# Kernel optimization log

Hardware: AMD Instinct MI355X
Metric: run time of the kernel (lower is better)

## Reference

```python
import jax, jax.numpy as jnp
import numpy as np

DIM = 1024
NUM_HEADS = 16


def setup_inputs() -> dict:
    key = jax.random.key(0)
    ks = jax.random.split(key, 5)
    B, Nx, Ny = 8, 1024, 1024
    w_std = DIM ** -0.5  # keep logits in a sane range
    x = jax.random.normal(ks[0], (B, Nx, DIM), dtype=jnp.float32)
    y = jax.random.normal(ks[1], (B, Ny, DIM), dtype=jnp.float32)
    Wq = jax.random.normal(ks[2], (DIM, DIM), dtype=jnp.float32) * w_std
    Wk = jax.random.normal(ks[3], (DIM, DIM), dtype=jnp.float32) * w_std
    Wv = jax.random.normal(ks[4], (DIM, DIM), dtype=jnp.float32) * w_std
    return {"x": x, "y": y, "Wq": Wq, "Wk": Wk, "Wv": Wv}


def reference(x, y, Wq, Wk, Wv):
    B, Nx, dim = x.shape
    Ny = y.shape[1]
    H = NUM_HEADS
    hd = dim // H
    scale = jnp.asarray(hd ** 0.5, dtype=x.dtype)

    # torch nn.Linear: out = inp @ W.T
    Q = (x @ Wq.T) / scale                 # [B, Nx, dim]
    K = y @ Wk.T                           # [B, Ny, dim]
    V = y @ Wv.T                           # [B, Ny, dim]

    # split(last, hd) + cat(dim=0) == reshape heads to leading axis
    Qh = Q.reshape(B, Nx, H, hd)
    Kh = K.reshape(B, Ny, H, hd)
    Vh = V.reshape(B, Ny, H, hd)

    logits = jnp.einsum("bqhd,bkhd->bhqk", Qh, Kh)   # [B, H, Nx, Ny]
    A = jax.nn.softmax(logits, axis=-1)
    y_ = jnp.einsum("bhqk,bkhd->bqhd", A, Vh).reshape(B, Nx, dim)

    # second stage: x @ y_^T, scaled, softmax over queries (dim=-2)
    s = jnp.einsum("bqd,bkd->bqk", x, y_) / scale    # [B, Nx, Nx]
    return jax.nn.softmax(s, axis=-2)
```

## Files before the change

### kernel.cpp

```cpp
#include <hip/hip_runtime.h>

typedef unsigned short ushort_t;
typedef __attribute__((ext_vector_type(8))) short short8;
typedef __attribute__((ext_vector_type(4))) float f32x4;
typedef __attribute__((ext_vector_type(2))) unsigned uint2v;
typedef __attribute__((ext_vector_type(4))) unsigned uint4v;

#define DIM 1024
#define BATCH 8
#define NSEQ 1024
#define HEADS 16
#define HD 64

__device__ __forceinline__ ushort_t f2b(float f) {
    union { float f; unsigned u; } v; v.f = f;
    unsigned r = v.u + 0x7FFF + ((v.u >> 16) & 1);
    return (ushort_t)(r >> 16);
}

__device__ __forceinline__ unsigned cvtpk_bf16(float a, float b) {
    unsigned r;
    asm("v_cvt_pk_bf16_f32 %0, %1, %2" : "=v"(r) : "v"(a), "v"(b));
    return r;
}

__device__ __forceinline__ void g2l16(const void* g, void* l) {
    __builtin_amdgcn_global_load_lds(
        (const __attribute__((address_space(1))) void*)g,
        (__attribute__((address_space(3))) void*)l, 16, 0, 0);
}

__global__ __launch_bounds__(256) void conv_all(const float4* __restrict__ x,
                                                const float4* __restrict__ y,
                                                const float4* __restrict__ wq,
                                                const float4* __restrict__ wk,
                                                const float4* __restrict__ wv,
                                                short8* __restrict__ xb,
                                                short8* __restrict__ yb,
                                                short8* __restrict__ wqb,
                                                short8* __restrict__ wkb,
                                                short8* __restrict__ wvb) {
    int j = blockIdx.x;
    const float4* src; short8* dst; int base;
    if (j < 4096)      { src = x;  dst = xb;  base = j; }
    else if (j < 8192) { src = y;  dst = yb;  base = j - 4096; }
    else if (j < 8704) { src = wq; dst = wqb; base = j - 8192; }
    else if (j < 9216) { src = wk; dst = wkb; base = j - 8704; }
    else               { src = wv; dst = wvb; base = j - 9216; }
    int i = base * 256 + threadIdx.x;
    float4 a = src[i * 2], b = src[i * 2 + 1];
    short8 o;
    o[0] = (short)f2b(a.x); o[1] = (short)f2b(a.y);
    o[2] = (short)f2b(a.z); o[3] = (short)f2b(a.w);
    o[4] = (short)f2b(b.x); o[5] = (short)f2b(b.y);
    o[6] = (short)f2b(b.z); o[7] = (short)f2b(b.w);
    dst[i] = o;
}

template <typename OutT, int MODE, bool EXPOUT>
__global__ __launch_bounds__(256) void gemm_nt(const ushort_t* __restrict__ A,
                                               const ushort_t* __restrict__ B,
                                               OutT* __restrict__ C,
                                               long sA, long sB, long sC,
                                               float scale,
                                               float* __restrict__ partial) {
    __shared__ __align__(16) ushort_t As[128 * 64];
    __shared__ __align__(16) ushort_t Bs[128 * 64];
    const int tid = threadIdx.x;
    const int w = tid >> 6, l = tid & 63;
    const int wm = w >> 1, wn = w & 1;
    const int lo = l & 15, hi = l >> 4;

    int bx, by, bz;
    const int j = blockIdx.x;
    if constexpr (MODE == 1) { by = j & 63; bx = j >> 6; bz = 0; }
    else if constexpr (MODE == 2) { bx = j & 7; by = (j >> 3) & 7; bz = j >> 6; }
    else { bz = j & 7; bx = (j >> 3) & 7; by = j >> 6; }

    const long abase = (long)by * 128 * 1024 + (long)bz * sA;
    const long bbase = (long)bx * 128 * 1024 + (long)bz * sB;
    const char* Abytes = (const char*)A;
    const char* Bbytes = (const char*)B;

    f32x4 acc[4][4];
#pragma unroll
    for (int m = 0; m < 4; m++)
#pragma unroll
        for (int n = 0; n < 4; n++) acc[m][n] = (f32x4)0.f;

    for (int kt = 0; kt < 1024; kt += 64) {
#pragma unroll
        for (int i = 0; i < 4; i++) {
            int o16 = tid + i * 256;
            int row = o16 >> 3;
            int cb = (o16 & 7) * 16;
            int scb = cb ^ ((row & 7) << 4);
            g2l16(Abytes + (abase + (long)row * 1024 + kt) * 2 + scb,
                  (char*)As + o16 * 16);
            g2l16(Bbytes + (bbase + (long)row * 1024 + kt) * 2 + scb,
                  (char*)Bs + o16 * 16);
        }
        __syncthreads();
#pragma unroll
        for (int kc = 0; kc < 2; kc++) {
            short8 af[4], bfr[4];
#pragma unroll
            for (int m = 0; m < 4; m++) {
                int row = wm * 64 + m * 16 + lo;
                int cb = (kc * 64 + hi * 16) ^ ((row & 7) << 4);
                af[m] = *(const short8*)((const char*)As + row * 128 + cb);
            }
#pragma unroll
            for (int n = 0; n < 4; n++) {
                int row = wn * 64 + n * 16 + lo;
                int cb = (kc * 64 + hi * 16) ^ ((row & 7) << 4);
                bfr[n] = *(const short8*)((const char*)Bs + row * 128 + cb);
            }
            __builtin_amdgcn_s_setprio(1);
#pragma unroll
            for (int m = 0; m < 4; m++)
#pragma unroll
                for (int n = 0; n < 4; n++)
                    acc[m][n] = __builtin_amdgcn_mfma_f32_16x16x32_bf16(
                        af[m], bfr[n], acc[m][n], 0, 0, 0);
            __builtin_amdgcn_s_setprio(0);
        }
        __syncthreads();
    }

    const long cb0 = (long)bz * sC;
    if constexpr (EXPOUT) {
#pragma unroll
        for (int n = 0; n < 4; n++) {
            float csum = 0.f;
#pragma unroll
            for (int m = 0; m < 4; m++)
#pragma unroll
                for (int r = 0; r < 4; r++) {
                    long row = (long)by * 128 + wm * 64 + m * 16 + hi * 4 + r;
                    long col = (long)bx * 128 + wn * 64 + n * 16 + lo;
                    float e = exp2f(acc[m][n][r] * scale);
                    C[cb0 + row * 1024 + col] = (OutT)e;
                    csum += e;
                }
            csum += __shfl_xor(csum, 16);
            csum += __shfl_xor(csum, 32);
            if (hi == 0)
                partial[((long)bz << 14) + (by * 2 + wm) * 1024 +
                        bx * 128 + wn * 64 + n * 16 + lo] = csum;
        }
    } else {
#pragma unroll
        for (int m = 0; m < 4; m++)
#pragma unroll
            for (int n = 0; n < 4; n++)
#pragma unroll
                for (int r = 0; r < 4; r++) {
                    long row = (long)by * 128 + wm * 64 + m * 16 + hi * 4 + r;
                    long col = (long)bx * 128 + wn * 64 + n * 16 + lo;
                    float v = acc[m][n][r] * scale;
                    if constexpr (sizeof(OutT) == 2)
                        C[cb0 + row * 1024 + col] = (OutT)f2b(v);
                    else
                        C[cb0 + row * 1024 + col] = v;
                }
    }
}

__global__ __launch_bounds__(256, 4) void flash_attn(const ushort_t* __restrict__ Q,
                                                     const ushort_t* __restrict__ Kb,
                                                     const ushort_t* __restrict__ Vt,
                                                     ushort_t* __restrict__ Yo) {
    __shared__ __align__(16) ushort_t Ks[2][64 * 64];
    __shared__ __align__(16) ushort_t Vs[2][64 * 64];
    const int j = blockIdx.x;
    const int g = j & 127, qt = j >> 7;
    const int h = g & 15, b = g >> 4;
    const int tid = threadIdx.x, w = tid >> 6, l = tid & 63;
    const int lo = l & 15, hi = l >> 4;
    const int sw = (lo & 7) << 4;

    const char* Khb = (const char*)(Kb + (long)b * 1024 * 1024 + h * 64);
    const char* Vhb = (const char*)(Vt + (long)b * 1024 * 1024 + (long)h * 64 * 1024);

    const long qrow0 = (long)b * 1024 + qt * 128 + w * 32;
    short8 qf[2][2];
#pragma unroll
    for (int qg = 0; qg < 2; qg++)
#pragma unroll
        for (int dk = 0; dk < 2; dk++)
            qf[qg][dk] = *(const short8*)(Q + (qrow0 + qg * 16 + lo) * 1024 +
                                          h * 64 + dk * 32 + hi * 8);

    float l_sum[2] = {0.f, 0.f};
    f32x4 o_acc[4][2];
#pragma unroll
    for (int ch = 0; ch < 4; ch++)
#pragma unroll
        for (int qg = 0; qg < 2; qg++) o_acc[ch][qg] = (f32x4)0.f;

    {
#pragma unroll
        for (int i = 0; i < 2; i++) {
            int o16 = tid + i * 256;
            int row = o16 >> 3, cb = (o16 & 7) * 16;
            int scb = cb ^ ((row & 7) << 4);
            g2l16(Khb + (long)row * 2048 + scb, (char*)Ks[0] + o16 * 16);
            g2l16(Vhb + (long)row * 2048 + scb, (char*)Vs[0] + o16 * 16);
        }
    }

    for (int t = 0; t < 16; t++) {
        __syncthreads();
        if (t < 15) {
            int kt = (t + 1) * 64;
            int bufn = (t + 1) & 1;
#pragma unroll
            for (int i = 0; i < 2; i++) {
                int o16 = tid + i * 256;
                int row = o16 >> 3, cb = (o16 & 7) * 16;
                int scb = cb ^ ((row & 7) << 4);
                g2l16(Khb + ((long)(kt + row) * 1024) * 2 + scb,
                      (char*)Ks[bufn] + o16 * 16);
                g2l16(Vhb + ((long)row * 1024 + kt) * 2 + scb,
                      (char*)Vs[bufn] + o16 * 16);
            }
        }
        const char* Kc = (const char*)Ks[t & 1];
        const char* Vc = (const char*)Vs[t & 1];

        f32x4 s_acc[4][2];
        __builtin_amdgcn_s_setprio(1);
#pragma unroll
        for (int ks = 0; ks < 4; ks++) {
            const char* kr = Kc + (ks * 16 + lo) * 128;
            short8 kf0 = *(const short8*)(kr + ((hi * 16) ^ sw));
            short8 kf1 = *(const short8*)(kr + ((64 + hi * 16) ^ sw));
#pragma unroll
            for (int qg = 0; qg < 2; qg++) {
                s_acc[ks][qg] = __builtin_amdgcn_mfma_f32_16x16x32_bf16(
                    kf0, qf[qg][0], (f32x4)0.f, 0, 0, 0);
                s_acc[ks][qg] = __builtin_amdgcn_mfma_f32_16x16x32_bf16(
                    kf1, qf[qg][1], s_acc[ks][qg], 0, 0, 0);
            }
        }
        __builtin_amdgcn_s_setprio(0);

        unsigned pk[2][4][2];
#pragma unroll
        for (int qg = 0; qg < 2; qg++) {
            float psk[4];
#pragma unroll
            for (int ks = 0; ks < 4; ks++) {
#pragma unroll
                for (int r = 0; r < 4; r++)
                    s_acc[ks][qg][r] = exp2f(s_acc[ks][qg][r]);
                psk[ks] = (s_acc[ks][qg][0] + s_acc[ks][qg][1]) +
                          (s_acc[ks][qg][2] + s_acc[ks][qg][3]);
                pk[qg][ks][0] = cvtpk_bf16(s_acc[ks][qg][0], s_acc[ks][qg][1]);
                pk[qg][ks][1] = cvtpk_bf16(s_acc[ks][qg][2], s_acc[ks][qg][3]);
            }
            float ps = (psk[0] + psk[1]) + (psk[2] + psk[3]);
            ps += __shfl_xor(ps, 16);
            ps += __shfl_xor(ps, 32);
            l_sum[qg] += ps;
        }

#pragma unroll
        for (int kk = 0; kk < 2; kk++) {
            short8 pa[2];
#pragma unroll
            for (int qg = 0; qg < 2; qg++) {
                unsigned a0 = pk[qg][2 * kk][0], b0 = pk[qg][2 * kk + 1][0];
                uint2v t0 = __builtin_amdgcn_permlane32_swap(a0, b0, false, false);
                t0 = __builtin_amdgcn_permlane16_swap(t0[0], t0[1], false, false);
                unsigned a1 = pk[qg][2 * kk][1], b1 = pk[qg][2 * kk + 1][1];
                uint2v t1 = __builtin_amdgcn_permlane32_swap(a1, b1, false, false);
                t1 = __builtin_amdgcn_permlane16_swap(t1[0], t1[1], false, false);
                union { uint4v u; short8 s; } cv;
                cv.u = (uint4v){t0[0], t1[0], t0[1], t1[1]};
                pa[qg] = cv.s;
            }
            __builtin_amdgcn_s_setprio(1);
#pragma unroll
            for (int ch = 0; ch < 4; ch++) {
                short8 vf = *(const short8*)(Vc + (ch * 16 + lo) * 128 +
                                             ((kk * 64 + hi * 16) ^ sw));
#pragma unroll
                for (int qg = 0; qg < 2; qg++)
                    o_acc[ch][qg] = __builtin_amdgcn_mfma_f32_16x16x32_bf16(
                        pa[qg], vf, o_acc[ch][qg], 0, 0, 0);
            }
            __builtin_amdgcn_s_setprio(0);
        }
    }

    float inv[2][4];
#pragma unroll
    for (int qg = 0; qg < 2; qg++)
#pragma unroll
        for (int r = 0; r < 4; r++)
            inv[qg][r] = 1.f / __shfl(l_sum[qg], hi * 4 + r);
#pragma unroll
    for (int ch = 0; ch < 4; ch++)
#pragma unroll
        for (int qg = 0; qg < 2; qg++)
#pragma unroll
            for (int r = 0; r < 4; r++) {
                long row = qrow0 + qg * 16 + hi * 4 + r;
                Yo[row * 1024 + h * 64 + ch * 16 + lo] =
                    f2b(o_acc[ch][qg][r] * inv[qg][r]);
            }
}

__global__ __launch_bounds__(256) void colsum_inv(const float* __restrict__ partial,
                                                  float* __restrict__ inv) {
    int i = blockIdx.x * 256 + threadIdx.x;
    int b = i >> 10, c = i & 1023;
    const float* p = partial + ((long)b << 14) + c;
    float s = 0.f;
#pragma unroll
    for (int k = 0; k < 16; k++) s += p[k * 1024];
    inv[i] = 1.f / s;
}

__global__ __launch_bounds__(256) void scale_rows(float4* __restrict__ S,
                                                  const float4* __restrict__ inv) {
    long i = (long)blockIdx.x * 256 + threadIdx.x;
    int c4 = (int)(i & 255);
    int b = (int)(i >> 18);
    float4 v = S[i];
    float4 iv = inv[b * 256 + c4];
    v.x *= iv.x; v.y *= iv.y; v.z *= iv.z; v.w *= iv.w;
    S[i] = v;
}

extern "C" void kernel_launch(void* const* d_in, const int* in_sizes, int n_in,
                              void* d_out, int out_size, void* d_ws, size_t ws_size,
                              hipStream_t stream) {
    const float* x = (const float*)d_in[0];
    const float* y = (const float*)d_in[1];
    const float* Wq = (const float*)d_in[2];
    const float* Wk = (const float*)d_in[3];
    const float* Wv = (const float*)d_in[4];
    float* out = (float*)d_out;

    const long NXD = (long)BATCH * NSEQ * DIM;
    const long WSZ = (long)DIM * DIM;
    ushort_t* xb = (ushort_t*)d_ws;
    ushort_t* yb = xb + NXD;
    ushort_t* wqb = yb + NXD;
    ushort_t* wkb = wqb + WSZ;
    ushort_t* wvb = wkb + WSZ;
    ushort_t* Qb = wvb + WSZ;
    ushort_t* Kbb = Qb + NXD;
    ushort_t* Vtb = Kbb + NXD;
    ushort_t* Yob = Vtb + NXD;
    float* partial = (float*)(Yob + NXD);
    float* invcol = partial + 8 * 16 * 1024;

    conv_all<<<9728, 256, 0, stream>>>((const float4*)x, (const float4*)y,
                                       (const float4*)Wq, (const float4*)Wk,
                                       (const float4*)Wv, (short8*)xb, (short8*)yb,
                                       (short8*)wqb, (short8*)wkb, (short8*)wvb);

    gemm_nt<ushort_t, 1, false><<<512, 256, 0, stream>>>(
        xb, wqb, Qb, 0, 0, 0, 0.125f * 1.44269504f, nullptr);
    gemm_nt<ushort_t, 1, false><<<512, 256, 0, stream>>>(
        yb, wkb, Kbb, 0, 0, 0, 1.0f, nullptr);
    gemm_nt<ushort_t, 2, false><<<512, 256, 0, stream>>>(
        wvb, yb, Vtb, 0, WSZ, WSZ, 1.0f, nullptr);
    flash_attn<<<1024, 256, 0, stream>>>(Qb, Kbb, Vtb, Yob);
    gemm_nt<float, 3, true><<<512, 256, 0, stream>>>(
        xb, Yob, out, WSZ, WSZ, WSZ, 0.125f * 1.44269504f, partial);
    colsum_inv<<<32, 256, 0, stream>>>(partial, invcol);
    scale_rows<<<8192, 256, 0, stream>>>((float4*)out, (const float4*)invcol);
}
```

Baseline: 281.5 us.

## Fuse column-softmax normalization into final GEMM via cross-block counters; MFMA row sums

```diff
diff --git a/kernel.cpp b/kernel.cpp
--- a/kernel.cpp
+++ b/kernel.cpp
@@ -39,8 +39,10 @@
                                                 short8* __restrict__ yb,
                                                 short8* __restrict__ wqb,
                                                 short8* __restrict__ wkb,
-                                                short8* __restrict__ wvb) {
+                                                short8* __restrict__ wvb,
+                                                int* __restrict__ counters) {
     int j = blockIdx.x;
+    if (j == 0 && threadIdx.x < 64) counters[threadIdx.x] = 0;
     const float4* src; short8* dst; int base;
     if (j < 4096)      { src = x;  dst = xb;  base = j; }
     else if (j < 8192) { src = y;  dst = yb;  base = j - 4096; }
@@ -63,7 +65,8 @@
                                                OutT* __restrict__ C,
                                                long sA, long sB, long sC,
                                                float scale,
-                                               float* __restrict__ partial) {
+                                               float* __restrict__ partial,
+                                               int* __restrict__ counters) {
     __shared__ __align__(16) ushort_t As[128 * 64];
     __shared__ __align__(16) ushort_t Bs[128 * 64];
     const int tid = threadIdx.x;
@@ -137,10 +140,8 @@
             for (int m = 0; m < 4; m++)
 #pragma unroll
                 for (int r = 0; r < 4; r++) {
-                    long row = (long)by * 128 + wm * 64 + m * 16 + hi * 4 + r;
-                    long col = (long)bx * 128 + wn * 64 + n * 16 + lo;
                     float e = exp2f(acc[m][n][r] * scale);
-                    C[cb0 + row * 1024 + col] = (OutT)e;
+                    acc[m][n][r] = e;
                     csum += e;
                 }
             csum += __shfl_xor(csum, 16);
@@ -149,6 +150,43 @@
                 partial[((long)bz << 14) + (by * 2 + wm) * 1024 +
                         bx * 128 + wn * 64 + n * 16 + lo] = csum;
         }
+        __threadfence();
+        __syncthreads();
+        const int g = bz * 8 + bx;
+        if (tid == 0) {
+            atomicAdd(&counters[g], 1);
+            while (atomicAdd(&counters[g], 0) < 8) __builtin_amdgcn_s_sleep(2);
+        }
+        __syncthreads();
+        __threadfence();
+        float* red = (float*)As;
+#pragma unroll
+        for (int i = 0; i < 8; i++) {
+            int idx = tid * 8 + i;
+            int k = idx >> 7, c = idx & 127;
+            red[idx] = partial[((long)bz << 14) + k * 1024 + bx * 128 + c];
+        }
+        __syncthreads();
+        if (tid < 128) {
+            float s = 0.f;
+#pragma unroll
+            for (int k = 0; k < 16; k++) s += red[k * 128 + tid];
+            red[2048 + tid] = 1.f / s;
+        }
+        __syncthreads();
+        float iv[4];
+#pragma unroll
+        for (int n = 0; n < 4; n++) iv[n] = red[2048 + wn * 64 + n * 16 + lo];
+#pragma unroll
+        for (int m = 0; m < 4; m++)
+#pragma unroll
+            for (int n = 0; n < 4; n++)
+#pragma unroll
+                for (int r = 0; r < 4; r++) {
+                    long row = (long)by * 128 + wm * 64 + m * 16 + hi * 4 + r;
+                    long col = (long)bx * 128 + wn * 64 + n * 16 + lo;
+                    C[cb0 + row * 1024 + col] = (OutT)(acc[m][n][r] * iv[n]);
+                }
     } else {
 #pragma unroll
         for (int m = 0; m < 4; m++)
@@ -192,12 +230,16 @@
             qf[qg][dk] = *(const short8*)(Q + (qrow0 + qg * 16 + lo) * 1024 +
                                           h * 64 + dk * 32 + hi * 8);
 
-    float l_sum[2] = {0.f, 0.f};
-    f32x4 o_acc[4][2];
+    short8 ones;
+#pragma unroll
+    for (int i = 0; i < 8; i++) ones[i] = (short)0x3F80;
+
+    f32x4 o_acc[4][2], o_sum[2];
 #pragma unroll
     for (int ch = 0; ch < 4; ch++)
 #pragma unroll
         for (int qg = 0; qg < 2; qg++) o_acc[ch][qg] = (f32x4)0.f;
+    o_sum[0] = (f32x4)0.f; o_sum[1] = (f32x4)0.f;
 
     {
 #pragma unroll
@@ -248,23 +290,15 @@
 
         unsigned pk[2][4][2];
 #pragma unroll
-        for (int qg = 0; qg < 2; qg++) {
-            float psk[4];
+        for (int qg = 0; qg < 2; qg++)
 #pragma unroll
             for (int ks = 0; ks < 4; ks++) {
 #pragma unroll
                 for (int r = 0; r < 4; r++)
                     s_acc[ks][qg][r] = exp2f(s_acc[ks][qg][r]);
-                psk[ks] = (s_acc[ks][qg][0] + s_acc[ks][qg][1]) +
-                          (s_acc[ks][qg][2] + s_acc[ks][qg][3]);
                 pk[qg][ks][0] = cvtpk_bf16(s_acc[ks][qg][0], s_acc[ks][qg][1]);
                 pk[qg][ks][1] = cvtpk_bf16(s_acc[ks][qg][2], s_acc[ks][qg][3]);
             }
-            float ps = (psk[0] + psk[1]) + (psk[2] + psk[3]);
-            ps += __shfl_xor(ps, 16);
-            ps += __shfl_xor(ps, 32);
-            l_sum[qg] += ps;
-        }
 
 #pragma unroll
         for (int kk = 0; kk < 2; kk++) {
@@ -283,6 +317,10 @@
             }
             __builtin_amdgcn_s_setprio(1);
 #pragma unroll
+            for (int qg = 0; qg < 2; qg++)
+                o_sum[qg] = __builtin_amdgcn_mfma_f32_16x16x32_bf16(
+                    pa[qg], ones, o_sum[qg], 0, 0, 0);
+#pragma unroll
             for (int ch = 0; ch < 4; ch++) {
                 short8 vf = *(const short8*)(Vc + (ch * 16 + lo) * 128 +
                                              ((kk * 64 + hi * 16) ^ sw));
@@ -300,7 +338,7 @@
     for (int qg = 0; qg < 2; qg++)
 #pragma unroll
         for (int r = 0; r < 4; r++)
-            inv[qg][r] = 1.f / __shfl(l_sum[qg], hi * 4 + r);
+            inv[qg][r] = 1.f / o_sum[qg][r];
 #pragma unroll
     for (int ch = 0; ch < 4; ch++)
 #pragma unroll
@@ -311,28 +349,6 @@
                 Yo[row * 1024 + h * 64 + ch * 16 + lo] =
                     f2b(o_acc[ch][qg][r] * inv[qg][r]);
             }
-}
-
-__global__ __launch_bounds__(256) void colsum_inv(const float* __restrict__ partial,
-                                                  float* __restrict__ inv) {
-    int i = blockIdx.x * 256 + threadIdx.x;
-    int b = i >> 10, c = i & 1023;
-    const float* p = partial + ((long)b << 14) + c;
-    float s = 0.f;
-#pragma unroll
-    for (int k = 0; k < 16; k++) s += p[k * 1024];
-    inv[i] = 1.f / s;
-}
-
-__global__ __launch_bounds__(256) void scale_rows(float4* __restrict__ S,
-                                                  const float4* __restrict__ inv) {
-    long i = (long)blockIdx.x * 256 + threadIdx.x;
-    int c4 = (int)(i & 255);
-    int b = (int)(i >> 18);
-    float4 v = S[i];
-    float4 iv = inv[b * 256 + c4];
-    v.x *= iv.x; v.y *= iv.y; v.z *= iv.z; v.w *= iv.w;
-    S[i] = v;
 }
 
 extern "C" void kernel_launch(void* const* d_in, const int* in_sizes, int n_in,
@@ -357,22 +373,21 @@
     ushort_t* Vtb = Kbb + NXD;
     ushort_t* Yob = Vtb + NXD;
     float* partial = (float*)(Yob + NXD);
-    float* invcol = partial + 8 * 16 * 1024;
+    int* counters = (int*)(partial + 8 * 16 * 1024);
 
     conv_all<<<9728, 256, 0, stream>>>((const float4*)x, (const float4*)y,
                                        (const float4*)Wq, (const float4*)Wk,
                                        (const float4*)Wv, (short8*)xb, (short8*)yb,
-                                       (short8*)wqb, (short8*)wkb, (short8*)wvb);
+                                       (short8*)wqb, (short8*)wkb, (short8*)wvb,
+                                       counters);
 
     gemm_nt<ushort_t, 1, false><<<512, 256, 0, stream>>>(
-        xb, wqb, Qb, 0, 0, 0, 0.125f * 1.44269504f, nullptr);
+        xb, wqb, Qb, 0, 0, 0, 0.125f * 1.44269504f, nullptr, nullptr);
     gemm_nt<ushort_t, 1, false><<<512, 256, 0, stream>>>(
-        yb, wkb, Kbb, 0, 0, 0, 1.0f, nullptr);
+        yb, wkb, Kbb, 0, 0, 0, 1.0f, nullptr, nullptr);
     gemm_nt<ushort_t, 2, false><<<512, 256, 0, stream>>>(
-        wvb, yb, Vtb, 0, WSZ, WSZ, 1.0f, nullptr);
+        wvb, yb, Vtb, 0, WSZ, WSZ, 1.0f, nullptr, nullptr);
     flash_attn<<<1024, 256, 0, stream>>>(Qb, Kbb, Vtb, Yob);
     gemm_nt<float, 3, true><<<512, 256, 0, stream>>>(
-        xb, Yob, out, WSZ, WSZ, WSZ, 0.125f * 1.44269504f, partial);
-    colsum_inv<<<32, 256, 0, stream>>>(partial, invcol);
-    scale_rows<<<8192, 256, 0, stream>>>((float4*)out, (const float4*)invcol);
-}
+        xb, Yob, out, WSZ, WSZ, WSZ, 0.125f * 1.44269504f, partial, counters);
+}
```

Result: slower. 334.3 us (+18.7%).

## Merge Q/K/V projections into one launch and compute softmax row sums via MFMA

Applied to the files above, without the earlier changes.

```diff
diff --git a/kernel.cpp b/kernel.cpp
--- a/kernel.cpp
+++ b/kernel.cpp
@@ -57,13 +57,15 @@
     dst[i] = o;
 }
 
-template <typename OutT, int MODE, bool EXPOUT>
-__global__ __launch_bounds__(256) void gemm_nt(const ushort_t* __restrict__ A,
-                                               const ushort_t* __restrict__ B,
-                                               OutT* __restrict__ C,
-                                               long sA, long sB, long sC,
-                                               float scale,
-                                               float* __restrict__ partial) {
+__global__ __launch_bounds__(256) void qkv_gemm(const ushort_t* __restrict__ xb,
+                                                const ushort_t* __restrict__ yb,
+                                                const ushort_t* __restrict__ wqb,
+                                                const ushort_t* __restrict__ wkb,
+                                                const ushort_t* __restrict__ wvb,
+                                                ushort_t* __restrict__ Qb,
+                                                ushort_t* __restrict__ Kbb,
+                                                ushort_t* __restrict__ Vtb,
+                                                float qscale) {
     __shared__ __align__(16) ushort_t As[128 * 64];
     __shared__ __align__(16) ushort_t Bs[128 * 64];
     const int tid = threadIdx.x;
@@ -71,14 +73,27 @@
     const int wm = w >> 1, wn = w & 1;
     const int lo = l & 15, hi = l >> 4;
 
-    int bx, by, bz;
     const int j = blockIdx.x;
-    if constexpr (MODE == 1) { by = j & 63; bx = j >> 6; bz = 0; }
-    else if constexpr (MODE == 2) { bx = j & 7; by = (j >> 3) & 7; bz = j >> 6; }
-    else { bz = j & 7; bx = (j >> 3) & 7; by = j >> 6; }
-
-    const long abase = (long)by * 128 * 1024 + (long)bz * sA;
-    const long bbase = (long)bx * 128 * 1024 + (long)bz * sB;
+    const ushort_t *A, *B;
+    ushort_t* C;
+    int bx, by;
+    long aoff = 0, boff = 0, coff = 0;
+    float scale;
+    if (j < 512) {
+        A = xb; B = wqb; C = Qb; by = j & 63; bx = j >> 6; scale = qscale;
+    } else if (j < 1024) {
+        int i = j - 512;
+        A = yb; B = wkb; C = Kbb; by = i & 63; bx = i >> 6; scale = 1.0f;
+    } else {
+        int i = j - 1024;
+        A = wvb; B = yb; C = Vtb; bx = i & 7; by = (i >> 3) & 7;
+        int bz = i >> 6;
+        boff = (long)bz * 1024 * 1024; coff = (long)bz * 1024 * 1024;
+        scale = 1.0f;
+    }
+
+    const long abase = (long)by * 128 * 1024 + aoff;
+    const long bbase = (long)bx * 128 * 1024 + boff;
     const char* Abytes = (const char*)A;
     const char* Bbytes = (const char*)B;
 
@@ -128,42 +143,103 @@
         __syncthreads();
     }
 
-    const long cb0 = (long)bz * sC;
-    if constexpr (EXPOUT) {
-#pragma unroll
-        for (int n = 0; n < 4; n++) {
-            float csum = 0.f;
+#pragma unroll
+    for (int m = 0; m < 4; m++)
+#pragma unroll
+        for (int n = 0; n < 4; n++)
+#pragma unroll
+            for (int r = 0; r < 4; r++) {
+                long row = (long)by * 128 + wm * 64 + m * 16 + hi * 4 + r;
+                long col = (long)bx * 128 + wn * 64 + n * 16 + lo;
+                C[coff + row * 1024 + col] = f2b(acc[m][n][r] * scale);
+            }
+}
+
+__global__ __launch_bounds__(256) void s_gemm(const ushort_t* __restrict__ A,
+                                              const ushort_t* __restrict__ B,
+                                              float* __restrict__ C,
+                                              float scale,
+                                              float* __restrict__ partial) {
+    __shared__ __align__(16) ushort_t As[128 * 64];
+    __shared__ __align__(16) ushort_t Bs[128 * 64];
+    const int tid = threadIdx.x;
+    const int w = tid >> 6, l = tid & 63;
+    const int wm = w >> 1, wn = w & 1;
+    const int lo = l & 15, hi = l >> 4;
+
+    const int j = blockIdx.x;
+    const int bz = j & 7, bx = (j >> 3) & 7, by = j >> 6;
+
+    const long abase = (long)by * 128 * 1024 + (long)bz * 1024 * 1024;
+    const long bbase = (long)bx * 128 * 1024 + (long)bz * 1024 * 1024;
+    const char* Abytes = (const char*)A;
+    const char* Bbytes = (const char*)B;
+
+    f32x4 acc[4][4];
+#pragma unroll
+    for (int m = 0; m < 4; m++)
+#pragma unroll
+        for (int n = 0; n < 4; n++) acc[m][n] = (f32x4)0.f;
+
+    for (int kt = 0; kt < 1024; kt += 64) {
+#pragma unroll
+        for (int i = 0; i < 4; i++) {
+            int o16 = tid + i * 256;
+            int row = o16 >> 3;
+            int cb = (o16 & 7) * 16;
+            int scb = cb ^ ((row & 7) << 4);
+            g2l16(Abytes + (abase + (long)row * 1024 + kt) * 2 + scb,
+                  (char*)As + o16 * 16);
+            g2l16(Bbytes + (bbase + (long)row * 1024 + kt) * 2 + scb,
+                  (char*)Bs + o16 * 16);
+        }
+        __syncthreads();
+#pragma unroll
+        for (int kc = 0; kc < 2; kc++) {
+            short8 af[4], bfr[4];
+#pragma unroll
+            for (int m = 0; m < 4; m++) {
+                int row = wm * 64 + m * 16 + lo;
+                int cb = (kc * 64 + hi * 16) ^ ((row & 7) << 4);
+                af[m] = *(const short8*)((const char*)As + row * 128 + cb);
+            }
+#pragma unroll
+            for (int n = 0; n < 4; n++) {
+                int row = wn * 64 + n * 16 + lo;
+                int cb = (kc * 64 + hi * 16) ^ ((row & 7) << 4);
+                bfr[n] = *(const short8*)((const char*)Bs + row * 128 + cb);
+            }
+            __builtin_amdgcn_s_setprio(1);
 #pragma unroll
             for (int m = 0; m < 4; m++)
 #pragma unroll
-                for (int r = 0; r < 4; r++) {
-                    long row = (long)by * 128 + wm * 64 + m * 16 + hi * 4 + r;
-                    long col = (long)bx * 128 + wn * 64 + n * 16 + lo;
-                    float e = exp2f(acc[m][n][r] * scale);
-                    C[cb0 + row * 1024 + col] = (OutT)e;
-                    csum += e;
-                }
-            csum += __shfl_xor(csum, 16);
-            csum += __shfl_xor(csum, 32);
-            if (hi == 0)
-                partial[((long)bz << 14) + (by * 2 + wm) * 1024 +
-                        bx * 128 + wn * 64 + n * 16 + lo] = csum;
-        }
-    } else {
+                for (int n = 0; n < 4; n++)
+                    acc[m][n] = __builtin_amdgcn_mfma_f32_16x16x32_bf16(
+                        af[m], bfr[n], acc[m][n], 0, 0, 0);
+            __builtin_amdgcn_s_setprio(0);
+        }
+        __syncthreads();
+    }
+
+    const long cb0 = (long)bz * 1024 * 1024;
+#pragma unroll
+    for (int n = 0; n < 4; n++) {
+        float csum = 0.f;
 #pragma unroll
         for (int m = 0; m < 4; m++)
 #pragma unroll
-            for (int n = 0; n < 4; n++)
-#pragma unroll
-                for (int r = 0; r < 4; r++) {
-                    long row = (long)by * 128 + wm * 64 + m * 16 + hi * 4 + r;
-                    long col = (long)bx * 128 + wn * 64 + n * 16 + lo;
-                    float v = acc[m][n][r] * scale;
-                    if constexpr (sizeof(OutT) == 2)
-                        C[cb0 + row * 1024 + col] = (OutT)f2b(v);
-                    else
-                        C[cb0 + row * 1024 + col] = v;
-                }
+            for (int r = 0; r < 4; r++) {
+                long row = (long)by * 128 + wm * 64 + m * 16 + hi * 4 + r;
+                long col = (long)bx * 128 + wn * 64 + n * 16 + lo;
+                float e = exp2f(acc[m][n][r] * scale);
+                C[cb0 + row * 1024 + col] = e;
+                csum += e;
+            }
+        csum += __shfl_xor(csum, 16);
+        csum += __shfl_xor(csum, 32);
+        if (hi == 0)
+            partial[((long)bz << 14) + (by * 2 + wm) * 1024 +
+                    bx * 128 + wn * 64 + n * 16 + lo] = csum;
     }
 }
 
@@ -192,12 +268,16 @@
             qf[qg][dk] = *(const short8*)(Q + (qrow0 + qg * 16 + lo) * 1024 +
                                           h * 64 + dk * 32 + hi * 8);
 
-    float l_sum[2] = {0.f, 0.f};
-    f32x4 o_acc[4][2];
+    short8 ones;
+#pragma unroll
+    for (int i = 0; i < 8; i++) ones[i] = (short)0x3F80;
+
+    f32x4 o_acc[4][2], o_sum[2];
 #pragma unroll
     for (int ch = 0; ch < 4; ch++)
 #pragma unroll
         for (int qg = 0; qg < 2; qg++) o_acc[ch][qg] = (f32x4)0.f;
+    o_sum[0] = (f32x4)0.f; o_sum[1] = (f32x4)0.f;
 
     {
 #pragma unroll
@@ -248,23 +328,15 @@
 
         unsigned pk[2][4][2];
 #pragma unroll
-        for (int qg = 0; qg < 2; qg++) {
-            float psk[4];
+        for (int qg = 0; qg < 2; qg++)
 #pragma unroll
             for (int ks = 0; ks < 4; ks++) {
 #pragma unroll
                 for (int r = 0; r < 4; r++)
                     s_acc[ks][qg][r] = exp2f(s_acc[ks][qg][r]);
-                psk[ks] = (s_acc[ks][qg][0] + s_acc[ks][qg][1]) +
-                          (s_acc[ks][qg][2] + s_acc[ks][qg][3]);
                 pk[qg][ks][0] = cvtpk_bf16(s_acc[ks][qg][0], s_acc[ks][qg][1]);
                 pk[qg][ks][1] = cvtpk_bf16(s_acc[ks][qg][2], s_acc[ks][qg][3]);
             }
-            float ps = (psk[0] + psk[1]) + (psk[2] + psk[3]);
-            ps += __shfl_xor(ps, 16);
-            ps += __shfl_xor(ps, 32);
-            l_sum[qg] += ps;
-        }
 
 #pragma unroll
         for (int kk = 0; kk < 2; kk++) {
@@ -283,6 +355,10 @@
             }
             __builtin_amdgcn_s_setprio(1);
 #pragma unroll
+            for (int qg = 0; qg < 2; qg++)
+                o_sum[qg] = __builtin_amdgcn_mfma_f32_16x16x32_bf16(
+                    pa[qg], ones, o_sum[qg], 0, 0, 0);
+#pragma unroll
             for (int ch = 0; ch < 4; ch++) {
                 short8 vf = *(const short8*)(Vc + (ch * 16 + lo) * 128 +
                                              ((kk * 64 + hi * 16) ^ sw));
@@ -300,7 +376,7 @@
     for (int qg = 0; qg < 2; qg++)
 #pragma unroll
         for (int r = 0; r < 4; r++)
-            inv[qg][r] = 1.f / __shfl(l_sum[qg], hi * 4 + r);
+            inv[qg][r] = 1.f / o_sum[qg][r];
 #pragma unroll
     for (int ch = 0; ch < 4; ch++)
 #pragma unroll
@@ -364,15 +440,10 @@
                                        (const float4*)Wv, (short8*)xb, (short8*)yb,
                                        (short8*)wqb, (short8*)wkb, (short8*)wvb);
 
-    gemm_nt<ushort_t, 1, false><<<512, 256, 0, stream>>>(
-        xb, wqb, Qb, 0, 0, 0, 0.125f * 1.44269504f, nullptr);
-    gemm_nt<ushort_t, 1, false><<<512, 256, 0, stream>>>(
-        yb, wkb, Kbb, 0, 0, 0, 1.0f, nullptr);
-    gemm_nt<ushort_t, 2, false><<<512, 256, 0, stream>>>(
-        wvb, yb, Vtb, 0, WSZ, WSZ, 1.0f, nullptr);
+    qkv_gemm<<<1536, 256, 0, stream>>>(xb, yb, wqb, wkb, wvb, Qb, Kbb, Vtb,
+                                       0.125f * 1.44269504f);
     flash_attn<<<1024, 256, 0, stream>>>(Qb, Kbb, Vtb, Yob);
-    gemm_nt<float, 3, true><<<512, 256, 0, stream>>>(
-        xb, Yob, out, WSZ, WSZ, WSZ, 0.125f * 1.44269504f, partial);
+    s_gemm<<<512, 256, 0, stream>>>(xb, Yob, out, 0.125f * 1.44269504f, partial);
     colsum_inv<<<32, 256, 0, stream>>>(partial, invcol);
     scale_rows<<<8192, 256, 0, stream>>>((float4*)out, (const float4*)invcol);
 }
```

Result: faster. 271.7 us (-3.5%).
